# Kernel tuning notes

Measured on AMD Instinct MI355X. Metric: run time of the kernel, lower is better.

Reference implementation:

```python
import jax, jax.numpy as jnp
import numpy as np

B, H, W, D = 16, 48, 48, 384
EPS = 1e-5


def setup_inputs() -> dict:
    key = jax.random.key(0)
    ks = jax.random.split(key, 7)
    s_in = 1.0 / np.sqrt(D)
    s_pos = 1.0 / np.sqrt(2.0)
    return {
        "x": jax.random.normal(ks[0], (B, H, W, D), dtype=jnp.float32),
        "Wp": jax.random.uniform(ks[1], (2, D), minval=-s_pos, maxval=s_pos, dtype=jnp.float32),
        "bp": jax.random.uniform(ks[2], (D,), minval=-s_pos, maxval=s_pos, dtype=jnp.float32),
        "W1": jax.random.uniform(ks[3], (D, D), minval=-s_in, maxval=s_in, dtype=jnp.float32),
        "b1": jax.random.uniform(ks[4], (D,), minval=-s_in, maxval=s_in, dtype=jnp.float32),
        "W2": jax.random.uniform(ks[5], (D, D), minval=-s_in, maxval=s_in, dtype=jnp.float32),
        "b2": jax.random.uniform(ks[6], (D,), minval=-s_in, maxval=s_in, dtype=jnp.float32),
    }


def reference(x, Wp, bp, W1, b1, W2, b2):
    b, h, w, d = x.shape
    # positional encoding: (h, w, 2) -> Linear(2, d)
    ph = jnp.arange(h, dtype=jnp.float32)[:, None] * jnp.ones((1, w), jnp.float32)
    pw = jnp.arange(w, dtype=jnp.float32)[None, :] * jnp.ones((h, 1), jnp.float32)
    pos = jnp.stack((ph, pw), axis=-1)  # (h, w, 2)
    pos_enc = pos @ Wp + bp  # (h, w, d)
    x = x + pos_enc[None]
    xf = x.reshape(b, h * w, d)
    # unscaled self-attention: softmax(x x^T) x
    scores = jnp.einsum("bnd,bmd->bnm", xf, xf)  # (b, hw, hw)
    attn = jax.nn.softmax(scores, axis=-1)
    out = jnp.einsum("bnm,bmd->bnd", attn, xf)  # (b, hw, d)
    # MLP: Linear -> ReLU -> Linear
    out = jax.nn.relu(out @ W1 + b1) @ W2 + b2
    out = out.reshape(b, h, w, d) + x
    # layer_norm over [h, w, d] (no affine params)
    mean = jnp.mean(out, axis=(1, 2, 3), keepdims=True)
    var = jnp.var(out, axis=(1, 2, 3), keepdims=True)
    return (out - mean) * jax.lax.rsqrt(var + EPS)
```

## Files before the change

### kernel.cpp

```cpp
#include <hip/hip_runtime.h>
#include <cstdio>
#include <cstdint>

#define BB 16
#define HH 48
#define WW 48
#define DD 384
#define NTOK 2304
#define EPS 1e-5f
#define SZB 28311552u

typedef __attribute__((ext_vector_type(4))) float f32x4;
typedef __attribute__((ext_vector_type(8))) short bf16x8;
typedef __attribute__((ext_vector_type(4))) short bf16x4;

__device__ __forceinline__ unsigned short f2bf(float f) {
  uint32_t u = __float_as_uint(f);
  uint32_t r = (u + 0x7FFFu + ((u >> 16) & 1u)) >> 16;
  return (unsigned short)r;
}
__device__ __forceinline__ float bf2f(short s) {
  return __uint_as_float(((uint32_t)(unsigned short)s) << 16);
}

typedef __attribute__((address_space(3))) uint32_t lds_u32;
typedef __attribute__((address_space(1))) const uint32_t glob_u32;
__device__ __forceinline__ void gload_lds16(const void* g, void* l) {
  __builtin_amdgcn_global_load_lds((glob_u32*)g, (lds_u32*)l, 16, 0, 0);
}

__global__ void k_prep(const float* __restrict__ x, const float* __restrict__ Wp,
                       const float* __restrict__ bp, short* __restrict__ xhi,
                       short* __restrict__ xlo, short* __restrict__ vfrag) {
  __shared__ __attribute__((aligned(16))) short tile[32 * 392];
  const int b = blockIdx.y, pt = blockIdx.x, tid = threadIdx.x;
  const int n0 = pt * 32;
  const float* src = x + ((size_t)b * NTOK + n0) * DD;
  short* hdst = xhi + ((size_t)b * NTOK + n0) * DD;
  short* ldst = xlo + ((size_t)b * NTOK + n0) * DD;
#pragma unroll
  for (int c = 0; c < 6; ++c) {
    int u = c * 256 + tid;
    int r = u / 48, c8 = u % 48;
    int d0 = c8 * 8;
    int n = n0 + r;
    float fh = (float)(n / WW), fw = (float)(n % WW);
    bf16x8 hv, lv;
#pragma unroll
    for (int j = 0; j < 8; ++j) {
      int d = d0 + j;
      float pe = fh * Wp[d] + fw * Wp[DD + d] + bp[d];
      float val = src[(size_t)r * DD + d] + pe;
      unsigned short hb = f2bf(val);
      hv[j] = (short)hb;
      lv[j] = (short)f2bf(val - bf2f((short)hb));
    }
    *(bf16x8*)(&tile[r * 392 + d0]) = hv;
    *(bf16x8*)(hdst + (size_t)r * DD + d0) = hv;
    *(bf16x8*)(ldst + (size_t)r * DD + d0) = lv;
  }
  __syncthreads();
  char* dst = (char*)vfrag + ((size_t)b * 72 + pt) * 24576;
#pragma unroll
  for (int c = 0; c < 6; ++c) {
    int u = c * 256 + tid;
    int db = u >> 6, l = u & 63, l15 = l & 15, lgv = l >> 4;
    bf16x8 vv;
#pragma unroll
    for (int j = 0; j < 8; ++j) {
      int tok = (j < 4) ? (lgv * 4 + j) : (16 + lgv * 4 + (j - 4));
      vv[j] = tile[tok * 392 + db * 16 + l15];
    }
    *(bf16x8*)(dst + (size_t)u * 16) = vv;
  }
}

__global__ void k_wprep(const float* __restrict__ W1, const float* __restrict__ W2,
                        short* __restrict__ w1t, short* __restrict__ w2t) {
  int idx = blockIdx.x * 256 + threadIdx.x;
  int r = idx / DD, c = idx % DD;
  w1t[c * DD + r] = (short)f2bf(W1[idx]);
  w2t[c * DD + r] = (short)f2bf(W2[idx]);
}

#define NTILE 144
#define NPAIR 72

__global__ __launch_bounds__(384, 2)
void k_attn(const short* __restrict__ xhi, const short* __restrict__ xlo,
            const short* __restrict__ vfrag, short* __restrict__ aout) {
  __shared__ __attribute__((aligned(16))) char lds_all[122880];
  const int tid = threadIdx.x;
  const int lane = tid & 63, wave = tid >> 6;
  const int ln15 = lane & 15, lg = lane >> 4;
  const int bid = blockIdx.x;
  const int xcd = bid & 7, slot = bid >> 3;
  const int half = (slot >= 24) ? 1 : 0;
  const int b = xcd + 8 * half;
  const int qt = slot - 24 * half;
  const int q0 = qt * 96;
  const int swz = (ln15 & 7) << 4;

  uint32_t srcoff[4];
#pragma unroll
  for (int c = 0; c < 4; ++c) {
    int g = c * 6144 + tid * 16;
    int region = (g >= 12288) ? 1 : 0;
    int rem = g - region * 12288;
    int row = rem / 768;
    int col = rem - row * 768;
    srcoff[c] = (uint32_t)(row * 768 + (col ^ ((row & 7) << 4))) + (region ? SZB : 0u);
  }
  const char* kbp = (const char*)xhi + (size_t)b * NTOK * 768;
  const char* vbp = (const char*)vfrag + (size_t)b * 1769472;

  bf16x8 qh[12], ql[12];
  {
    const short* qp = xhi + ((size_t)b * NTOK + q0 + wave * 16 + ln15) * DD + lg * 8;
    const short* qlp = xlo + ((size_t)b * NTOK + q0 + wave * 16 + ln15) * DD + lg * 8;
#pragma unroll
    for (int kf = 0; kf < 12; ++kf) {
      qh[kf] = *(const bf16x8*)(qp + kf * 32);
      ql[kf] = *(const bf16x8*)(qlp + kf * 32);
    }
  }

  f32x4 o[24];
#pragma unroll
  for (int i = 0; i < 24; ++i) o[i] = f32x4{0.f, 0.f, 0.f, 0.f};
  float m1 = -INFINITY, l1 = 0.0f;

  char* bA = lds_all;
  char* bB = lds_all + 24576;
  char* bC = lds_all + 49152;
  char* vA = lds_all + 73728;
  char* vB = lds_all + 98304;

#pragma unroll
  for (int c = 0; c < 4; ++c) gload_lds16(kbp + srcoff[c], bA + c * 6144 + tid * 16);
#pragma unroll
  for (int c = 0; c < 4; ++c) gload_lds16(kbp + 12288 + srcoff[c], bB + c * 6144 + tid * 16);
#pragma unroll
  for (int c = 0; c < 4; ++c) gload_lds16(vbp + c * 6144 + tid * 16, vA + c * 6144 + tid * 16);
  asm volatile("s_waitcnt vmcnt(8)" ::: "memory");
  __builtin_amdgcn_s_barrier();
  __builtin_amdgcn_sched_barrier(0);

#pragma unroll 1
  for (int p = 0; p < NPAIR; ++p) {
    if (2 * p + 2 < NTILE) {
      const char* kn = kbp + (size_t)(2 * p + 2) * 12288;
#pragma unroll
      for (int c = 0; c < 4; ++c) gload_lds16(kn + srcoff[c], bC + c * 6144 + tid * 16);
    }
    f32x4 shh = f32x4{0.f, 0.f, 0.f, 0.f}, shl = shh, slh = shh;
    __builtin_amdgcn_s_setprio(1);
#pragma unroll
    for (int kf = 0; kf < 12; ++kf) {
      const int ca = (kf * 64 + lg * 16) ^ swz;
      bf16x8 ah = *(const bf16x8*)(bA + ln15 * 768 + ca);
      bf16x8 al = *(const bf16x8*)(bA + 12288 + ln15 * 768 + ca);
      shh = __builtin_amdgcn_mfma_f32_16x16x32_bf16(ah, qh[kf], shh, 0, 0, 0);
      shl = __builtin_amdgcn_mfma_f32_16x16x32_bf16(ah, ql[kf], shl, 0, 0, 0);
      slh = __builtin_amdgcn_mfma_f32_16x16x32_bf16(al, qh[kf], slh, 0, 0, 0);
    }
    __builtin_amdgcn_s_setprio(0);
    f32x4 sE;
#pragma unroll
    for (int r = 0; r < 4; ++r) sE[r] = shh[r] + shl[r] + slh[r];

    if (p + 1 < NPAIR) {
      asm volatile("s_waitcnt vmcnt(4)" ::: "memory");
    } else {
      asm volatile("s_waitcnt vmcnt(0)" ::: "memory");
    }
    __builtin_amdgcn_s_barrier();
    __builtin_amdgcn_sched_barrier(0);

    if (2 * p + 3 < NTILE) {
      const char* kn = kbp + (size_t)(2 * p + 3) * 12288;
#pragma unroll
      for (int c = 0; c < 4; ++c) gload_lds16(kn + srcoff[c], bA + c * 6144 + tid * 16);
    }
    if (p + 1 < NPAIR) {
      const char* vn = vbp + (size_t)(p + 1) * 24576;
#pragma unroll
      for (int c = 0; c < 4; ++c) gload_lds16(vn + c * 6144 + tid * 16, vB + c * 6144 + tid * 16);
    }
    shh = f32x4{0.f, 0.f, 0.f, 0.f}; shl = shh; slh = shh;
    __builtin_amdgcn_s_setprio(1);
#pragma unroll
    for (int kf = 0; kf < 12; ++kf) {
      const int ca = (kf * 64 + lg * 16) ^ swz;
      bf16x8 ah = *(const bf16x8*)(bB + ln15 * 768 + ca);
      bf16x8 al = *(const bf16x8*)(bB + 12288 + ln15 * 768 + ca);
      shh = __builtin_amdgcn_mfma_f32_16x16x32_bf16(ah, qh[kf], shh, 0, 0, 0);
      shl = __builtin_amdgcn_mfma_f32_16x16x32_bf16(ah, ql[kf], shl, 0, 0, 0);
      slh = __builtin_amdgcn_mfma_f32_16x16x32_bf16(al, qh[kf], slh, 0, 0, 0);
    }
    __builtin_amdgcn_s_setprio(0);
    f32x4 sO;
#pragma unroll
    for (int r = 0; r < 4; ++r) sO[r] = shh[r] + shl[r] + slh[r];

    float tmax = -INFINITY;
#pragma unroll
    for (int r = 0; r < 4; ++r) tmax = fmaxf(tmax, fmaxf(sE[r], sO[r]));
    tmax = fmaxf(tmax, __shfl_xor(tmax, 16));
    tmax = fmaxf(tmax, __shfl_xor(tmax, 32));
    if (__any(tmax - m1 > 8.f)) {
      float mn = fmaxf(m1, tmax);
      float al_ = __expf(m1 - mn);
      float alr[4];
#pragma unroll
      for (int r = 0; r < 4; ++r) alr[r] = __shfl(al_, lg * 4 + r);
#pragma unroll
      for (int ob = 0; ob < 24; ++ob)
#pragma unroll
        for (int r = 0; r < 4; ++r) o[ob][r] *= alr[r];
      l1 *= al_;
      m1 = mn;
    }
    float rs = 0.0f;
    bf16x8 p8;
#pragma unroll
    for (int r = 0; r < 4; ++r) {
      float pe = __expf(sE[r] - m1);
      float po = __expf(sO[r] - m1);
      rs += pe + po;
      p8[r] = (short)f2bf(pe);
      p8[r + 4] = (short)f2bf(po);
    }
    rs += __shfl_xor(rs, 16);
    rs += __shfl_xor(rs, 32);
    l1 += rs;

    const char* vt = vA + lane * 16;
    __builtin_amdgcn_s_setprio(1);
#pragma unroll
    for (int g = 0; g < 4; ++g) {
#pragma unroll
      for (int j = 0; j < 6; ++j) {
        bf16x8 vv = *(const bf16x8*)(vt + (g * 6 + j) * 1024);
        o[g * 6 + j] = __builtin_amdgcn_mfma_f32_16x16x32_bf16(p8, vv, o[g * 6 + j], 0, 0, 0);
      }
    }
    __builtin_amdgcn_s_setprio(0);

    asm volatile("s_waitcnt vmcnt(8)" ::: "memory");
    __builtin_amdgcn_s_barrier();
    __builtin_amdgcn_sched_barrier(0);

    char* t0 = bA;
    char* t1 = bB;
    bA = bC; bB = t0; bC = t1;
    char* tv = vA; vA = vB; vB = tv;
  }

  float lr[4];
#pragma unroll
  for (int r = 0; r < 4; ++r) lr[r] = __shfl(l1, lg * 4 + r);
  short* ob_ = aout + ((size_t)b * NTOK + q0 + wave * 16) * DD;
#pragma unroll
  for (int db = 0; db < 24; ++db) {
#pragma unroll
    for (int r = 0; r < 4; ++r) {
      float v = o[db][r] / lr[r];
      ob_[(size_t)(lg * 4 + r) * DD + db * 16 + ln15] = (short)f2bf(v);
    }
  }
}

__global__ __launch_bounds__(128, 3)
void k_mlp(const short* __restrict__ aout, const short* __restrict__ w1t,
           const short* __restrict__ w2t, const float* __restrict__ b1,
           const float* __restrict__ b2, const short* __restrict__ xhi,
           const short* __restrict__ xlo, short* __restrict__ ybf,
           float* __restrict__ stats) {
  __shared__ __attribute__((aligned(16))) short hid[2 * 16 * 392];
  __shared__ float redS[2], redQ[2];
  const int tid = threadIdx.x, lane = tid & 63, wave = tid >> 6;
  const int ln15 = lane & 15, lg = lane >> 4;
  const int row0 = blockIdx.x * 32;
  const int bb = row0 / NTOK;

  bf16x8 a[12];
  {
    const short* ap = aout + (size_t)(row0 + wave * 16 + ln15) * DD + lg * 8;
#pragma unroll
    for (int kf = 0; kf < 12; ++kf) a[kf] = *(const bf16x8*)(ap + kf * 32);
  }
  short* hw = &hid[wave * 16 * 392];
#pragma unroll 1
  for (int cb = 0; cb < 24; ++cb) {
    f32x4 acc = f32x4{0.f, 0.f, 0.f, 0.f};
#pragma unroll
    for (int kf = 0; kf < 12; ++kf) {
      bf16x8 wf = *(const bf16x8*)(w1t + (size_t)(cb * 16 + ln15) * DD + kf * 32 + lg * 8);
      acc = __builtin_amdgcn_mfma_f32_16x16x32_bf16(a[kf], wf, acc, 0, 0, 0);
    }
    float bias = b1[cb * 16 + ln15];
#pragma unroll
    for (int r = 0; r < 4; ++r) {
      float v = fmaxf(acc[r] + bias, 0.0f);
      hw[(lg * 4 + r) * 392 + cb * 16 + ln15] = (short)f2bf(v);
    }
  }
  __syncthreads();
  bf16x8 h[12];
#pragma unroll
  for (int kf = 0; kf < 12; ++kf)
    h[kf] = *(const bf16x8*)(&hw[ln15 * 392 + kf * 32 + lg * 8]);
  float ts = 0.f, tq = 0.f;
#pragma unroll 1
  for (int cb = 0; cb < 24; ++cb) {
    f32x4 acc = f32x4{0.f, 0.f, 0.f, 0.f};
#pragma unroll
    for (int kf = 0; kf < 12; ++kf) {
      bf16x8 wf = *(const bf16x8*)(w2t + (size_t)(cb * 16 + ln15) * DD + kf * 32 + lg * 8);
      acc = __builtin_amdgcn_mfma_f32_16x16x32_bf16(h[kf], wf, acc, 0, 0, 0);
    }
    int col = cb * 16 + ln15;
    float bias = b2[col];
#pragma unroll
    for (int r = 0; r < 4; ++r) {
      size_t row = (size_t)row0 + wave * 16 + lg * 4 + r;
      size_t idx = row * DD + col;
      float xv = bf2f(xhi[idx]) + bf2f(xlo[idx]);
      float y = acc[r] + bias + xv;
      ybf[idx] = (short)f2bf(y);
      ts += y;
      tq += y * y;
    }
  }
#pragma unroll
  for (int off = 32; off; off >>= 1) {
    ts += __shfl_xor(ts, off);
    tq += __shfl_xor(tq, off);
  }
  if (lane == 0) { redS[wave] = ts; redQ[wave] = tq; }
  __syncthreads();
  if (tid == 0) {
    atomicAdd(&stats[bb], redS[0] + redS[1]);
    atomicAdd(&stats[16 + bb], redQ[0] + redQ[1]);
  }
}

__global__ void k_ln(const short* __restrict__ ybf, float* __restrict__ out,
                     const float* __restrict__ stats) {
  size_t i8 = ((size_t)blockIdx.x * 256 + threadIdx.x) * 8;
  int b = (int)(i8 / ((size_t)NTOK * DD));
  const float cnt = (float)(NTOK * DD);
  float mean = stats[b] / cnt;
  float var = stats[16 + b] / cnt - mean * mean;
  float inv = rsqrtf(var + EPS);
  bf16x8 v = *(const bf16x8*)(ybf + i8);
  f32x4 o0, o1;
#pragma unroll
  for (int j = 0; j < 4; ++j) {
    o0[j] = (bf2f(v[j]) - mean) * inv;
    o1[j] = (bf2f(v[j + 4]) - mean) * inv;
  }
  *(f32x4*)(out + i8) = o0;
  *(f32x4*)(out + i8 + 4) = o1;
}

extern "C" void kernel_launch(void* const* d_in, const int* in_sizes, int n_in,
                              void* d_out, int out_size, void* d_ws, size_t ws_size,
                              hipStream_t stream) {
  const float* x  = (const float*)d_in[0];
  const float* Wp = (const float*)d_in[1];
  const float* bp = (const float*)d_in[2];
  const float* W1 = (const float*)d_in[3];
  const float* b1 = (const float*)d_in[4];
  const float* W2 = (const float*)d_in[5];
  const float* b2 = (const float*)d_in[6];
  float* out = (float*)d_out;

  const size_t SZ = (size_t)SZB;
  char* ws = (char*)d_ws;
  short* xhi   = (short*)ws;
  short* xlo   = (short*)(ws + SZ);
  short* vfrag = (short*)(ws + 2 * SZ);
  short* aout  = (short*)(ws + 3 * SZ);
  short* w1t   = (short*)(ws + 4 * SZ);
  short* w2t   = (short*)(ws + 4 * SZ + 294912);
  float* stats = (float*)(ws + 4 * SZ + 2 * 294912);
  const size_t need = 4 * SZ + 2 * 294912 + 128;
  if (ws_size < need) {
    fprintf(stderr, "kernel_launch: ws_size %zu < needed %zu\n", ws_size, need);
  }

  k_prep<<<dim3(72, 16), 256, 0, stream>>>(x, Wp, bp, xhi, xlo, vfrag);
  k_wprep<<<576, 256, 0, stream>>>(W1, W2, w1t, w2t);
  k_attn<<<384, 384, 0, stream>>>(xhi, xlo, vfrag, aout);
  hipMemsetAsync(stats, 0, 32 * sizeof(float), stream);
  k_mlp<<<1152, 128, 0, stream>>>(aout, w1t, w2t, b1, b2, xhi, xlo, aout, stats);
  k_ln<<<6912, 256, 0, stream>>>(aout, out, stats);
}
```

Before: 665.2 us.

## Split attention into two launches to balance query tiles across CUs

The attention kernel is templated on wave count and launched twice. The first launch covers the first 1536 queries per batch with 96-query blocks, and the second covers the remaining 768 with 48-query, 3-wave blocks, each launch using 256 blocks. The old grid of 384 blocks left some CUs with two blocks and others with one; the new split aims to spread work evenly across CUs. The trade-off is only one block per CU in each launch, which gives less latency hiding. It also adds a second launch, and the 3-wave variant needs more loads per thread, so its wait counts change.

Result: slower. 679.0 us (+2.1%).

```diff
diff --git a/kernel.cpp b/kernel.cpp
--- a/kernel.cpp
+++ b/kernel.cpp
@@ -86,25 +86,27 @@
 #define NTILE 144
 #define NPAIR 72
 
-__global__ __launch_bounds__(384, 2)
+template <int NW>
+__global__ __launch_bounds__(NW * 64, 2)
 void k_attn(const short* __restrict__ xhi, const short* __restrict__ xlo,
-            const short* __restrict__ vfrag, short* __restrict__ aout) {
+            const short* __restrict__ vfrag, short* __restrict__ aout, int qbase) {
+  constexpr int C = 24 / NW;
   __shared__ __attribute__((aligned(16))) char lds_all[122880];
   const int tid = threadIdx.x;
   const int lane = tid & 63, wave = tid >> 6;
   const int ln15 = lane & 15, lg = lane >> 4;
   const int bid = blockIdx.x;
   const int xcd = bid & 7, slot = bid >> 3;
-  const int half = (slot >= 24) ? 1 : 0;
+  const int half = (slot >= 16) ? 1 : 0;
   const int b = xcd + 8 * half;
-  const int qt = slot - 24 * half;
-  const int q0 = qt * 96;
+  const int qt = slot - 16 * half;
+  const int q0 = qbase + qt * (NW * 16);
   const int swz = (ln15 & 7) << 4;
 
-  uint32_t srcoff[4];
-#pragma unroll
-  for (int c = 0; c < 4; ++c) {
-    int g = c * 6144 + tid * 16;
+  uint32_t srcoff[C];
+#pragma unroll
+  for (int c = 0; c < C; ++c) {
+    int g = c * (NW * 1024) + tid * 16;
     int region = (g >= 12288) ? 1 : 0;
     int rem = g - region * 12288;
     int row = rem / 768;
@@ -113,6 +115,7 @@
   }
   const char* kbp = (const char*)xhi + (size_t)b * NTOK * 768;
   const char* vbp = (const char*)vfrag + (size_t)b * 1769472;
+  const int dofs = tid * 16;
 
   bf16x8 qh[12], ql[12];
   {
@@ -137,12 +140,13 @@
   char* vB = lds_all + 98304;
 
 #pragma unroll
-  for (int c = 0; c < 4; ++c) gload_lds16(kbp + srcoff[c], bA + c * 6144 + tid * 16);
-#pragma unroll
-  for (int c = 0; c < 4; ++c) gload_lds16(kbp + 12288 + srcoff[c], bB + c * 6144 + tid * 16);
-#pragma unroll
-  for (int c = 0; c < 4; ++c) gload_lds16(vbp + c * 6144 + tid * 16, vA + c * 6144 + tid * 16);
-  asm volatile("s_waitcnt vmcnt(8)" ::: "memory");
+  for (int c = 0; c < C; ++c) gload_lds16(kbp + srcoff[c], bA + c * (NW * 1024) + dofs);
+#pragma unroll
+  for (int c = 0; c < C; ++c) gload_lds16(kbp + 12288 + srcoff[c], bB + c * (NW * 1024) + dofs);
+#pragma unroll
+  for (int c = 0; c < C; ++c) gload_lds16(vbp + c * (NW * 1024) + dofs, vA + c * (NW * 1024) + dofs);
+  if constexpr (NW == 6) asm volatile("s_waitcnt vmcnt(8)" ::: "memory");
+  else                   asm volatile("s_waitcnt vmcnt(16)" ::: "memory");
   __builtin_amdgcn_s_barrier();
   __builtin_amdgcn_sched_barrier(0);
 
@@ -151,7 +155,7 @@
     if (2 * p + 2 < NTILE) {
       const char* kn = kbp + (size_t)(2 * p + 2) * 12288;
 #pragma unroll
-      for (int c = 0; c < 4; ++c) gload_lds16(kn + srcoff[c], bC + c * 6144 + tid * 16);
+      for (int c = 0; c < C; ++c) gload_lds16(kn + srcoff[c], bC + c * (NW * 1024) + dofs);
     }
     f32x4 shh = f32x4{0.f, 0.f, 0.f, 0.f}, shl = shh, slh = shh;
     __builtin_amdgcn_s_setprio(1);
@@ -170,7 +174,8 @@
     for (int r = 0; r < 4; ++r) sE[r] = shh[r] + shl[r] + slh[r];
 
     if (p + 1 < NPAIR) {
-      asm volatile("s_waitcnt vmcnt(4)" ::: "memory");
+      if constexpr (NW == 6) asm volatile("s_waitcnt vmcnt(4)" ::: "memory");
+      else                   asm volatile("s_waitcnt vmcnt(8)" ::: "memory");
     } else {
       asm volatile("s_waitcnt vmcnt(0)" ::: "memory");
     }
@@ -180,12 +185,12 @@
     if (2 * p + 3 < NTILE) {
       const char* kn = kbp + (size_t)(2 * p + 3) * 12288;
 #pragma unroll
-      for (int c = 0; c < 4; ++c) gload_lds16(kn + srcoff[c], bA + c * 6144 + tid * 16);
+      for (int c = 0; c < C; ++c) gload_lds16(kn + srcoff[c], bA + c * (NW * 1024) + dofs);
     }
     if (p + 1 < NPAIR) {
       const char* vn = vbp + (size_t)(p + 1) * 24576;
 #pragma unroll
-      for (int c = 0; c < 4; ++c) gload_lds16(vn + c * 6144 + tid * 16, vB + c * 6144 + tid * 16);
+      for (int c = 0; c < C; ++c) gload_lds16(vn + c * (NW * 1024) + dofs, vB + c * (NW * 1024) + dofs);
     }
     shh = f32x4{0.f, 0.f, 0.f, 0.f}; shl = shh; slh = shh;
     __builtin_amdgcn_s_setprio(1);
@@ -247,7 +252,8 @@
     }
     __builtin_amdgcn_s_setprio(0);
 
-    asm volatile("s_waitcnt vmcnt(8)" ::: "memory");
+    if constexpr (NW == 6) asm volatile("s_waitcnt vmcnt(8)" ::: "memory");
+    else                   asm volatile("s_waitcnt vmcnt(16)" ::: "memory");
     __builtin_amdgcn_s_barrier();
     __builtin_amdgcn_sched_barrier(0);
 
@@ -393,7 +399,8 @@
 
   k_prep<<<dim3(72, 16), 256, 0, stream>>>(x, Wp, bp, xhi, xlo, vfrag);
   k_wprep<<<576, 256, 0, stream>>>(W1, W2, w1t, w2t);
-  k_attn<<<384, 384, 0, stream>>>(xhi, xlo, vfrag, aout);
+  k_attn<6><<<256, 384, 0, stream>>>(xhi, xlo, vfrag, aout, 0);
+  k_attn<3><<<256, 192, 0, stream>>>(xhi, xlo, vfrag, aout, 1536);
   hipMemsetAsync(stats, 0, 32 * sizeof(float), stream);
   k_mlp<<<1152, 128, 0, stream>>>(aout, w1t, w2t, b1, b2, xhi, xlo, aout, stats);
   k_ln<<<6912, 256, 0, stream>>>(aout, out, stats);
```

## Split attention KV range in two halves and merge partials in combine kernel

Applied to the files above, without the earlier changes.

Each attention block now handles half of the key/value tiles, which doubles the grid from 384 to 768 blocks. Each half writes unnormalized bf16 partial outputs plus its running max and sum, and a new combine kernel rescales and merges the two halves into the attention output. The goal is better occupancy: 384 blocks at 2 per CU left many CUs underused. In exchange it adds an extra kernel, extra global traffic for the partials, and a second bf16 rounding of the unnormalized output. The second partial buffer reuses the output buffer as scratch.

Result: faster. 578.7 us (-13.0%).

```diff
diff --git a/kernel.cpp b/kernel.cpp
--- a/kernel.cpp
+++ b/kernel.cpp
@@ -83,22 +83,23 @@
   w2t[c * DD + r] = (short)f2bf(W2[idx]);
 }
 
-#define NTILE 144
-#define NPAIR 72
-
 __global__ __launch_bounds__(384, 2)
 void k_attn(const short* __restrict__ xhi, const short* __restrict__ xlo,
-            const short* __restrict__ vfrag, short* __restrict__ aout) {
+            const short* __restrict__ vfrag, short* __restrict__ o1out,
+            short* __restrict__ o2out, float* __restrict__ ml) {
   __shared__ __attribute__((aligned(16))) char lds_all[122880];
   const int tid = threadIdx.x;
   const int lane = tid & 63, wave = tid >> 6;
   const int ln15 = lane & 15, lg = lane >> 4;
   const int bid = blockIdx.x;
-  const int xcd = bid & 7, slot = bid >> 3;
-  const int half = (slot >= 24) ? 1 : 0;
-  const int b = xcd + 8 * half;
-  const int qt = slot - 24 * half;
+  const int xcd = bid & 7, s = bid >> 3;
+  const int bh = (s >= 48) ? 1 : 0;
+  const int b = xcd + 8 * bh;
+  const int s2 = s - 48 * bh;
+  const int h = s2 / 24;
+  const int qt = s2 % 24;
   const int q0 = qt * 96;
+  const int pair0 = h * 36, pair1 = pair0 + 36;
   const int swz = (ln15 & 7) << 4;
 
   uint32_t srcoff[4];
@@ -113,6 +114,7 @@
   }
   const char* kbp = (const char*)xhi + (size_t)b * NTOK * 768;
   const char* vbp = (const char*)vfrag + (size_t)b * 1769472;
+  const int dofs = tid * 16;
 
   bf16x8 qh[12], ql[12];
   {
@@ -136,22 +138,26 @@
   char* vA = lds_all + 73728;
   char* vB = lds_all + 98304;
 
-#pragma unroll
-  for (int c = 0; c < 4; ++c) gload_lds16(kbp + srcoff[c], bA + c * 6144 + tid * 16);
-#pragma unroll
-  for (int c = 0; c < 4; ++c) gload_lds16(kbp + 12288 + srcoff[c], bB + c * 6144 + tid * 16);
-#pragma unroll
-  for (int c = 0; c < 4; ++c) gload_lds16(vbp + c * 6144 + tid * 16, vA + c * 6144 + tid * 16);
+  {
+    const char* kt = kbp + (size_t)(2 * pair0) * 12288;
+    const char* vt0 = vbp + (size_t)pair0 * 24576;
+#pragma unroll
+    for (int c = 0; c < 4; ++c) gload_lds16(kt + srcoff[c], bA + c * 6144 + dofs);
+#pragma unroll
+    for (int c = 0; c < 4; ++c) gload_lds16(kt + 12288 + srcoff[c], bB + c * 6144 + dofs);
+#pragma unroll
+    for (int c = 0; c < 4; ++c) gload_lds16(vt0 + c * 6144 + dofs, vA + c * 6144 + dofs);
+  }
   asm volatile("s_waitcnt vmcnt(8)" ::: "memory");
   __builtin_amdgcn_s_barrier();
   __builtin_amdgcn_sched_barrier(0);
 
 #pragma unroll 1
-  for (int p = 0; p < NPAIR; ++p) {
-    if (2 * p + 2 < NTILE) {
+  for (int p = pair0; p < pair1; ++p) {
+    if (2 * p + 2 < 2 * pair1) {
       const char* kn = kbp + (size_t)(2 * p + 2) * 12288;
 #pragma unroll
-      for (int c = 0; c < 4; ++c) gload_lds16(kn + srcoff[c], bC + c * 6144 + tid * 16);
+      for (int c = 0; c < 4; ++c) gload_lds16(kn + srcoff[c], bC + c * 6144 + dofs);
     }
     f32x4 shh = f32x4{0.f, 0.f, 0.f, 0.f}, shl = shh, slh = shh;
     __builtin_amdgcn_s_setprio(1);
@@ -169,7 +175,7 @@
 #pragma unroll
     for (int r = 0; r < 4; ++r) sE[r] = shh[r] + shl[r] + slh[r];
 
-    if (p + 1 < NPAIR) {
+    if (p + 1 < pair1) {
       asm volatile("s_waitcnt vmcnt(4)" ::: "memory");
     } else {
       asm volatile("s_waitcnt vmcnt(0)" ::: "memory");
@@ -177,15 +183,15 @@
     __builtin_amdgcn_s_barrier();
     __builtin_amdgcn_sched_barrier(0);
 
-    if (2 * p + 3 < NTILE) {
+    if (2 * p + 3 < 2 * pair1) {
       const char* kn = kbp + (size_t)(2 * p + 3) * 12288;
 #pragma unroll
-      for (int c = 0; c < 4; ++c) gload_lds16(kn + srcoff[c], bA + c * 6144 + tid * 16);
-    }
-    if (p + 1 < NPAIR) {
+      for (int c = 0; c < 4; ++c) gload_lds16(kn + srcoff[c], bA + c * 6144 + dofs);
+    }
+    if (p + 1 < pair1) {
       const char* vn = vbp + (size_t)(p + 1) * 24576;
 #pragma unroll
-      for (int c = 0; c < 4; ++c) gload_lds16(vn + c * 6144 + tid * 16, vB + c * 6144 + tid * 16);
+      for (int c = 0; c < 4; ++c) gload_lds16(vn + c * 6144 + dofs, vB + c * 6144 + dofs);
     }
     shh = f32x4{0.f, 0.f, 0.f, 0.f}; shl = shh; slh = shh;
     __builtin_amdgcn_s_setprio(1);
@@ -257,18 +263,36 @@
     char* tv = vA; vA = vB; vB = tv;
   }
 
-  float lr[4];
-#pragma unroll
-  for (int r = 0; r < 4; ++r) lr[r] = __shfl(l1, lg * 4 + r);
-  short* ob_ = aout + ((size_t)b * NTOK + q0 + wave * 16) * DD;
-#pragma unroll
-  for (int db = 0; db < 24; ++db) {
-#pragma unroll
-    for (int r = 0; r < 4; ++r) {
-      float v = o[db][r] / lr[r];
-      ob_[(size_t)(lg * 4 + r) * DD + db * 16 + ln15] = (short)f2bf(v);
-    }
-  }
+  short* ob_ = (h == 0 ? o1out : o2out) + ((size_t)b * NTOK + q0 + wave * 16) * DD;
+#pragma unroll
+  for (int db = 0; db < 24; ++db)
+#pragma unroll
+    for (int r = 0; r < 4; ++r)
+      ob_[(size_t)(lg * 4 + r) * DD + db * 16 + ln15] = (short)f2bf(o[db][r]);
+  if (lg == 0) {
+    float2 mv;
+    mv.x = m1;
+    mv.y = l1;
+    ((float2*)ml)[(size_t)h * (BB * NTOK) + (size_t)b * NTOK + q0 + wave * 16 + ln15] = mv;
+  }
+}
+
+__global__ void k_comb(const short* __restrict__ o1, const short* __restrict__ o2,
+                       const float* __restrict__ ml, short* __restrict__ aout) {
+  size_t i8 = ((size_t)blockIdx.x * 256 + threadIdx.x) * 8;
+  size_t row = i8 / DD;
+  float2 s1 = ((const float2*)ml)[row];
+  float2 s2 = ((const float2*)ml)[(size_t)BB * NTOK + row];
+  float m = fmaxf(s1.x, s2.x);
+  float a1 = __expf(s1.x - m), a2 = __expf(s2.x - m);
+  float inv = 1.0f / (a1 * s1.y + a2 * s2.y);
+  bf16x8 v1 = *(const bf16x8*)(o1 + i8);
+  bf16x8 v2 = *(const bf16x8*)(o2 + i8);
+  bf16x8 w;
+#pragma unroll
+  for (int j = 0; j < 8; ++j)
+    w[j] = (short)f2bf((a1 * bf2f(v1[j]) + a2 * bf2f(v2[j])) * inv);
+  *(bf16x8*)(aout + i8) = w;
 }
 
 __global__ __launch_bounds__(128, 3)
@@ -383,17 +407,20 @@
   short* xlo   = (short*)(ws + SZ);
   short* vfrag = (short*)(ws + 2 * SZ);
   short* aout  = (short*)(ws + 3 * SZ);
+  short* o2    = (short*)d_out;
   short* w1t   = (short*)(ws + 4 * SZ);
   short* w2t   = (short*)(ws + 4 * SZ + 294912);
   float* stats = (float*)(ws + 4 * SZ + 2 * 294912);
-  const size_t need = 4 * SZ + 2 * 294912 + 128;
+  float* ml    = (float*)(ws + 4 * SZ + 2 * 294912 + 256);
+  const size_t need = 4 * SZ + 2 * 294912 + 256 + 589824 + 128;
   if (ws_size < need) {
     fprintf(stderr, "kernel_launch: ws_size %zu < needed %zu\n", ws_size, need);
   }
 
   k_prep<<<dim3(72, 16), 256, 0, stream>>>(x, Wp, bp, xhi, xlo, vfrag);
   k_wprep<<<576, 256, 0, stream>>>(W1, W2, w1t, w2t);
-  k_attn<<<384, 384, 0, stream>>>(xhi, xlo, vfrag, aout);
+  k_attn<<<768, 384, 0, stream>>>(xhi, xlo, vfrag, aout, o2, ml);
+  k_comb<<<6912, 256, 0, stream>>>(aout, o2, ml, aout);
   hipMemsetAsync(stats, 0, 32 * sizeof(float), stream);
   k_mlp<<<1152, 128, 0, stream>>>(aout, w1t, w2t, b1, b2, xhi, xlo, aout, stats);
   k_ln<<<6912, 256, 0, stream>>>(aout, out, stats);
```
